# Performance work log

Measured on AMD Instinct MI355X. Metric: run time of the kernel, lower is better.

## Reference

```python
import jax, jax.numpy as jnp
import numpy as np

B, S, D = 4, 4096, 1024
H, HEAD_DIM = 16, 192  # head_dim split into q/k/v of 64 each


def setup_inputs() -> dict:
    key = jax.random.key(0)
    k1, k2 = jax.random.split(key)
    x = jax.random.normal(k1, (B, S, D), dtype=jnp.float32)
    qkv_kernel = jax.random.normal(k2, (D, H, HEAD_DIM), dtype=jnp.float32) * (1.0 / np.sqrt(D))
    qkv_bias = jnp.zeros((H, HEAD_DIM), dtype=jnp.float32)
    return {"x": x, "qkv_kernel": qkv_kernel, "qkv_bias": qkv_bias}


def reference(x, qkv_kernel, qkv_bias):
    # DenseGeneral: [B,S,D] x [D,H,HEAD_DIM] -> [B,S,H,HEAD_DIM]
    qkv = jnp.einsum('bsd,dhf->bshf', x, qkv_kernel) + qkv_bias
    q, k, v = jnp.split(qkv, 3, axis=-1)  # each [B,S,H,64]
    # Faithful to source layout: einsum '...hqd,...hkd' batches over (B,S) and
    # attends across the HEAD axis. With H <= block_size the blockwise loop in
    # the source collapses to this single full softmax over heads.
    scale = 1.0 / jnp.sqrt(jnp.asarray(HEAD_DIM, dtype=q.dtype))  # sqrt(self.head_dim)
    scores = jnp.einsum('bshd,bsgd->bshg', q, k) * scale  # [B,S,H,H]
    weights = jax.nn.softmax(scores, axis=-1)
    out = jnp.einsum('bshg,bsgd->bshd', weights, v)  # [B,S,H,64]
    return out
```

## Files before the change

### kernel.cpp

```cpp
#include <hip/hip_runtime.h>
#include <cstdint>
#include <cstddef>

typedef unsigned short u16;
typedef __attribute__((ext_vector_type(8))) short bf16x8;
typedef __attribute__((ext_vector_type(4))) float f32x4;

__device__ inline float bl(uint32_t u){ union{float f;uint32_t i;}c; c.i = u<<16; return c.f; }
__device__ inline float bh(uint32_t u){ union{float f;uint32_t i;}c; c.i = u & 0xFFFF0000u; return c.f; }
__device__ inline u16 f2bu(float f){
  union{float f;uint32_t u;} c; c.f=f;
  uint32_t u=c.u;
  return (u16)((u + 0x7FFFu + ((u>>16)&1u))>>16);
}

#define GLOAD_LDS16(g, l) __builtin_amdgcn_global_load_lds( \
    (__attribute__((address_space(1))) void*)(g), \
    (__attribute__((address_space(3))) void*)(l), 16, 0, 0)
#define BAR() do{ asm volatile("" ::: "memory"); __builtin_amdgcn_s_barrier(); asm volatile("" ::: "memory"); }while(0)

__global__ __launch_bounds__(256) void k_conv(const float* __restrict__ X,
                                              u16* __restrict__ Xb,
                                              const float* __restrict__ W,
                                              u16* __restrict__ Wt){
  __shared__ float t[32][33];
  int b = blockIdx.x;
  if (b < 2048){
    int i = b*256 + threadIdx.x;
    for (; i < 4194304; i += 2048*256){
      float4 v = ((const float4*)X)[i];
      ushort4 o;
      o.x=f2bu(v.x); o.y=f2bu(v.y); o.z=f2bu(v.z); o.w=f2bu(v.w);
      ((ushort4*)Xb)[i] = o;
    }
  } else {
    int bb = b - 2048;
    int n0 = (bb % 96)*32, k0 = (bb / 96)*32;
    int tx = threadIdx.x & 31, ty = threadIdx.x >> 5;
    #pragma unroll
    for (int i=0;i<32;i+=8)
      t[ty+i][tx] = W[(size_t)(k0+ty+i)*3072 + n0+tx];
    __syncthreads();
    #pragma unroll
    for (int i=0;i<32;i+=8)
      Wt[(size_t)(n0+ty+i)*1024 + k0+tx] = f2bu(t[tx][ty+i]);
  }
}

__global__ __launch_bounds__(512, 2) void k_gemm2(const u16* __restrict__ Xb,
                                                  const u16* __restrict__ Wt,
                                                  const float* __restrict__ bias,
                                                  u16* __restrict__ Q){
  __shared__ __align__(16) u16 L[65536];
  const int K = 1024, N = 3072, NT = 32;
  int b = blockIdx.x;
  int swz = (b & 7)*96 + (b >> 3);
  int bm = swz / 12, bn = swz % 12;
  int m0 = bm*256, n0 = bn*256;
  int tid = threadIdx.x, w = tid>>6, lane = tid&63, lr = lane&15, lk = lane>>4;
  int wm = w>>2, wn = w&3;

  f32x4 acc[8][4];
  #pragma unroll
  for (int i=0;i<8;i++)
    #pragma unroll
    for (int j=0;j<4;j++)
      acc[i][j] = (f32x4){0.f,0.f,0.f,0.f};

  int grow = tid>>2;
  int gcol = ((((tid&3)*16) ^ (((tid>>3)&1)<<4) ^ (((tid>>4)&1)<<5)) >> 1);
  const u16* gA0 = Xb + (size_t)(m0 + grow)*K + gcol;
  const u16* gA1 = Xb + (size_t)(m0 + 128 + grow)*K + gcol;
  const u16* gB0 = Wt + (size_t)(n0 + grow)*K + gcol;
  const u16* gB1 = Wt + (size_t)(n0 + 128 + grow)*K + gcol;

#define STG_A(j) do{ int bf=(j)&3, kof=(j)*32; \
    GLOAD_LDS16(gA0+kof, &L[((bf*4+0)<<12) + tid*8]); \
    GLOAD_LDS16(gA1+kof, &L[((bf*4+1)<<12) + tid*8]); }while(0)
#define STG_B(j) do{ int bf=(j)&3, kof=(j)*32; \
    GLOAD_LDS16(gB0+kof, &L[((bf*4+2)<<12) + tid*8]); \
    GLOAD_LDS16(gB1+kof, &L[((bf*4+3)<<12) + tid*8]); }while(0)

  const char* Lb = (const char*)L;
  int colx = (lk*16) ^ (((lr>>1)&3)*16);
  int arow = lr*64 + colx;
  int brow = ((wn&1)*64 + lr)*64 + colx;

  STG_A(0); STG_B(0);
  STG_A(1); STG_B(1);
  STG_A(2); STG_B(2);
  asm volatile("s_waitcnt vmcnt(8)" ::: "memory");
  __builtin_amdgcn_sched_barrier(0);
  BAR();

  for (int t = 0; t < NT; ++t){
    int buf = t & 3;
    int Abase = (buf*4 + wm) << 13;
    int Bbase = (buf*4 + 2 + (wn>>1)) << 13;
    bool st = (t <= NT-4);
    if (st) { STG_A(t+3); STG_B(t+3); }

    bf16x8 a0,a1,a2,a3,a4,a5,a6,a7, b0,b1,b2,b3;
    a0 = *(const bf16x8*)(Lb + Abase + 0*1024 + arow);
    a1 = *(const bf16x8*)(Lb + Abase + 1*1024 + arow);
    a2 = *(const bf16x8*)(Lb + Abase + 2*1024 + arow);
    a3 = *(const bf16x8*)(Lb + Abase + 3*1024 + arow);
    a4 = *(const bf16x8*)(Lb + Abase + 4*1024 + arow);
    a5 = *(const bf16x8*)(Lb + Abase + 5*1024 + arow);
    a6 = *(const bf16x8*)(Lb + Abase + 6*1024 + arow);
    a7 = *(const bf16x8*)(Lb + Abase + 7*1024 + arow);
    b0 = *(const bf16x8*)(Lb + Bbase + 0*1024 + brow);
    b1 = *(const bf16x8*)(Lb + Bbase + 1*1024 + brow);
    b2 = *(const bf16x8*)(Lb + Bbase + 2*1024 + brow);
    b3 = *(const bf16x8*)(Lb + Bbase + 3*1024 + brow);

    __builtin_amdgcn_s_setprio(1);
    acc[0][0] = __builtin_amdgcn_mfma_f32_16x16x32_bf16(a0, b0, acc[0][0], 0,0,0);
    acc[0][1] = __builtin_amdgcn_mfma_f32_16x16x32_bf16(a0, b1, acc[0][1], 0,0,0);
    acc[0][2] = __builtin_amdgcn_mfma_f32_16x16x32_bf16(a0, b2, acc[0][2], 0,0,0);
    acc[0][3] = __builtin_amdgcn_mfma_f32_16x16x32_bf16(a0, b3, acc[0][3], 0,0,0);
    acc[1][0] = __builtin_amdgcn_mfma_f32_16x16x32_bf16(a1, b0, acc[1][0], 0,0,0);
    acc[1][1] = __builtin_amdgcn_mfma_f32_16x16x32_bf16(a1, b1, acc[1][1], 0,0,0);
    acc[1][2] = __builtin_amdgcn_mfma_f32_16x16x32_bf16(a1, b2, acc[1][2], 0,0,0);
    acc[1][3] = __builtin_amdgcn_mfma_f32_16x16x32_bf16(a1, b3, acc[1][3], 0,0,0);
    acc[2][0] = __builtin_amdgcn_mfma_f32_16x16x32_bf16(a2, b0, acc[2][0], 0,0,0);
    acc[2][1] = __builtin_amdgcn_mfma_f32_16x16x32_bf16(a2, b1, acc[2][1], 0,0,0);
    acc[2][2] = __builtin_amdgcn_mfma_f32_16x16x32_bf16(a2, b2, acc[2][2], 0,0,0);
    acc[2][3] = __builtin_amdgcn_mfma_f32_16x16x32_bf16(a2, b3, acc[2][3], 0,0,0);
    acc[3][0] = __builtin_amdgcn_mfma_f32_16x16x32_bf16(a3, b0, acc[3][0], 0,0,0);
    acc[3][1] = __builtin_amdgcn_mfma_f32_16x16x32_bf16(a3, b1, acc[3][1], 0,0,0);
    acc[3][2] = __builtin_amdgcn_mfma_f32_16x16x32_bf16(a3, b2, acc[3][2], 0,0,0);
    acc[3][3] = __builtin_amdgcn_mfma_f32_16x16x32_bf16(a3, b3, acc[3][3], 0,0,0);
    acc[4][0] = __builtin_amdgcn_mfma_f32_16x16x32_bf16(a4, b0, acc[4][0], 0,0,0);
    acc[4][1] = __builtin_amdgcn_mfma_f32_16x16x32_bf16(a4, b1, acc[4][1], 0,0,0);
    acc[4][2] = __builtin_amdgcn_mfma_f32_16x16x32_bf16(a4, b2, acc[4][2], 0,0,0);
    acc[4][3] = __builtin_amdgcn_mfma_f32_16x16x32_bf16(a4, b3, acc[4][3], 0,0,0);
    acc[5][0] = __builtin_amdgcn_mfma_f32_16x16x32_bf16(a5, b0, acc[5][0], 0,0,0);
    acc[5][1] = __builtin_amdgcn_mfma_f32_16x16x32_bf16(a5, b1, acc[5][1], 0,0,0);
    acc[5][2] = __builtin_amdgcn_mfma_f32_16x16x32_bf16(a5, b2, acc[5][2], 0,0,0);
    acc[5][3] = __builtin_amdgcn_mfma_f32_16x16x32_bf16(a5, b3, acc[5][3], 0,0,0);
    acc[6][0] = __builtin_amdgcn_mfma_f32_16x16x32_bf16(a6, b0, acc[6][0], 0,0,0);
    acc[6][1] = __builtin_amdgcn_mfma_f32_16x16x32_bf16(a6, b1, acc[6][1], 0,0,0);
    acc[6][2] = __builtin_amdgcn_mfma_f32_16x16x32_bf16(a6, b2, acc[6][2], 0,0,0);
    acc[6][3] = __builtin_amdgcn_mfma_f32_16x16x32_bf16(a6, b3, acc[6][3], 0,0,0);
    acc[7][0] = __builtin_amdgcn_mfma_f32_16x16x32_bf16(a7, b0, acc[7][0], 0,0,0);
    acc[7][1] = __builtin_amdgcn_mfma_f32_16x16x32_bf16(a7, b1, acc[7][1], 0,0,0);
    acc[7][2] = __builtin_amdgcn_mfma_f32_16x16x32_bf16(a7, b2, acc[7][2], 0,0,0);
    acc[7][3] = __builtin_amdgcn_mfma_f32_16x16x32_bf16(a7, b3, acc[7][3], 0,0,0);
    __builtin_amdgcn_s_setprio(0);

    asm volatile("s_waitcnt lgkmcnt(0)" ::: "memory");
    if (t <= NT-4)      { asm volatile("s_waitcnt vmcnt(8)" ::: "memory"); }
    else if (t == NT-3) { asm volatile("s_waitcnt vmcnt(4)" ::: "memory"); }
    else if (t == NT-2) { asm volatile("s_waitcnt vmcnt(0)" ::: "memory"); }
    __builtin_amdgcn_sched_barrier(0);
    BAR();
  }
#undef STG_A
#undef STG_B

  {
    u16* reg = &L[w*8192];
    #pragma unroll
    for (int nf=0; nf<4; ++nf){
      int col = nf*16 + lr;
      float bv = bias[n0 + wn*64 + col];
      #pragma unroll
      for (int mi=0; mi<8; ++mi){
        #pragma unroll
        for (int r=0;r<4;r++){
          int rr = mi*16 + lk*4 + r;
          reg[rr*64 + (col ^ ((rr&7)<<3))] = f2bu(acc[mi][nf][r] + bv);
        }
      }
    }
    asm volatile("s_waitcnt lgkmcnt(0)" ::: "memory");
    BAR();
    int co = (tid&31)*8;
    int rgn_c = co>>6;
    int c6 = co&63;
    #pragma unroll
    for (int p=0; p<16; ++p){
      int rI = p*16 + (tid>>5);
      int wreg = ((rI>>7)<<2) + rgn_c;
      int rr = rI & 127;
      const u16* src = &L[wreg*8192 + rr*64 + (c6 ^ ((rr&7)<<3))];
      uint4 v = *(const uint4*)src;
      *(uint4*)&Q[(size_t)(m0+rI)*N + n0 + co] = v;
    }
  }
}

__device__ inline void load16fb(const u16* p, float* f){
  uint4 a = ((const uint4*)p)[0], b4 = ((const uint4*)p)[1];
  f[0]=bl(a.x);  f[1]=bh(a.x);  f[2]=bl(a.y);  f[3]=bh(a.y);
  f[4]=bl(a.z);  f[5]=bh(a.z);  f[6]=bl(a.w);  f[7]=bh(a.w);
  f[8]=bl(b4.x); f[9]=bh(b4.x); f[10]=bl(b4.y);f[11]=bh(b4.y);
  f[12]=bl(b4.z);f[13]=bh(b4.z);f[14]=bl(b4.w);f[15]=bh(b4.w);
}

__global__ __launch_bounds__(256) void k_attn(const u16* __restrict__ Qkv,
                                              float* __restrict__ out){
  __shared__ __align__(16) u16 sm[4][3072];
  int w = threadIdx.x>>6, lane = threadIdx.x&63;
  int token = blockIdx.x*4 + w;
  const uint4* src = (const uint4*)(Qkv + (size_t)token*3072);
  uint4* dst = (uint4*)&sm[w][0];
  for (int i = lane; i < 384; i += 64) dst[i] = src[i];
  __syncthreads();

  int h = lane>>2, dq = lane&3;
  const u16* base = &sm[w][0];
  float qf[16];
  load16fb(base + h*192 + dq*16, qf);

  const float scale = 0.07216878364870323f;
  float s[16];
  #pragma unroll
  for (int g=0; g<16; ++g){
    float kf[16];
    load16fb(base + g*192 + 64 + dq*16, kf);
    float a = 0.f;
    #pragma unroll
    for (int j=0;j<16;j++) a += qf[j]*kf[j];
    a += __shfl_xor(a, 1);
    a += __shfl_xor(a, 2);
    s[g] = a * scale;
  }
  float mx = s[0];
  #pragma unroll
  for (int g=1; g<16; ++g) mx = fmaxf(mx, s[g]);
  float sum = 0.f;
  #pragma unroll
  for (int g=0; g<16; ++g){ s[g] = __expf(s[g]-mx); sum += s[g]; }
  float inv = 1.f/sum;

  float o[16];
  #pragma unroll
  for (int j=0;j<16;j++) o[j] = 0.f;
  #pragma unroll
  for (int g=0; g<16; ++g){
    float wg = s[g]*inv;
    float vf[16];
    load16fb(base + g*192 + 128 + dq*16, vf);
    #pragma unroll
    for (int j=0;j<16;j++) o[j] += wg*vf[j];
  }
  float* op = out + (size_t)token*1024 + h*64 + dq*16;
  #pragma unroll
  for (int i=0;i<4;i++)
    ((float4*)op)[i] = make_float4(o[i*4], o[i*4+1], o[i*4+2], o[i*4+3]);
}

__global__ __launch_bounds__(256) void k_fallback(const float* __restrict__ X,
                                                  const float* __restrict__ W,
                                                  const float* __restrict__ bias,
                                                  float* __restrict__ out){
  int token = blockIdx.x;
  __shared__ float xs[1024];
  __shared__ float qkvs[3072];
  __shared__ float ss[16][16];
  __shared__ float ww[16][16];
  for (int i=threadIdx.x; i<1024; i+=256) xs[i] = X[(size_t)token*1024 + i];
  __syncthreads();
  for (int n=threadIdx.x; n<3072; n+=256){
    float acc = bias[n];
    for (int k=0;k<1024;k++) acc += xs[k]*W[(size_t)k*3072 + n];
    qkvs[n] = acc;
  }
  __syncthreads();
  {
    int t = threadIdx.x, h = t>>4, g = t&15;
    float a = 0.f;
    for (int d=0; d<64; d++) a += qkvs[h*192 + d]*qkvs[g*192 + 64 + d];
    ss[h][g] = a * 0.07216878364870323f;
  }
  __syncthreads();
  if (threadIdx.x < 16){
    int hh = threadIdx.x;
    float m = -1e30f;
    for (int g=0;g<16;g++) m = fmaxf(m, ss[hh][g]);
    float sum = 0.f;
    for (int g=0;g<16;g++){ float e = __expf(ss[hh][g]-m); ww[hh][g]=e; sum+=e; }
    float inv = 1.f/sum;
    for (int g=0;g<16;g++) ww[hh][g] *= inv;
  }
  __syncthreads();
  for (int i=threadIdx.x; i<1024; i+=256){
    int h = i>>6, d = i&63;
    float a = 0.f;
    for (int g=0;g<16;g++) a += ww[h][g]*qkvs[g*192 + 128 + d];
    out[(size_t)token*1024 + i] = a;
  }
}

extern "C" void kernel_launch(void* const* d_in, const int* in_sizes, int n_in,
                              void* d_out, int out_size, void* d_ws, size_t ws_size,
                              hipStream_t stream){
  const float* x    = (const float*)d_in[0];
  const float* wk   = (const float*)d_in[1];
  const float* bias = (const float*)d_in[2];
  float* out = (float*)d_out;

  const size_t offW = 33554432;
  const size_t offQ = offW + 6291456;
  const size_t need = offQ + (size_t)16384*3072*2;

  if (ws_size >= need){
    u16* Xb = (u16*)d_ws;
    u16* Wt = (u16*)((char*)d_ws + offW);
    u16* Q  = (u16*)((char*)d_ws + offQ);
    k_conv  <<<5120, 256, 0, stream>>>(x, Xb, wk, Wt);
    k_gemm2 <<<768, 512, 0, stream>>>(Xb, Wt, bias, Q);
    k_attn  <<<4096, 256, 0, stream>>>(Q, out);
  } else {
    k_fallback<<<16384, 256, 0, stream>>>(x, wk, bias, out);
  }
}
```

Measured before the change: 191.9 us.

## Deepen GEMM LDS ring to five stages and process two k-tiles per barrier

The LDS staging ring grows from four to five buffers, and A/B loads merge into a single STG macro. The main loop is unrolled by two, so each barrier and waitcnt now covers two k-tiles instead of one, with the prefetch distance kept at three to four tiles ahead. This halves the number of workgroup barriers and lets more loads stay in flight. In exchange, LDS usage rises to 160KB and launch bounds drop to one block per CU, which gives the compiler more register freedom but leaves no room for a second resident block.

```diff
diff --git a/kernel.cpp b/kernel.cpp
--- a/kernel.cpp
+++ b/kernel.cpp
@@ -47,11 +47,11 @@
   }
 }
 
-__global__ __launch_bounds__(512, 2) void k_gemm2(const u16* __restrict__ Xb,
+__global__ __launch_bounds__(512, 1) void k_gemm2(const u16* __restrict__ Xb,
                                                   const u16* __restrict__ Wt,
                                                   const float* __restrict__ bias,
                                                   u16* __restrict__ Q){
-  __shared__ __align__(16) u16 L[65536];
+  __shared__ __align__(16) u16 L[81920];
   const int K = 1024, N = 3072, NT = 32;
   int b = blockIdx.x;
   int swz = (b & 7)*96 + (b >> 3);
@@ -74,10 +74,9 @@
   const u16* gB0 = Wt + (size_t)(n0 + grow)*K + gcol;
   const u16* gB1 = Wt + (size_t)(n0 + 128 + grow)*K + gcol;
 
-#define STG_A(j) do{ int bf=(j)&3, kof=(j)*32; \
+#define STG(j) do{ int bf=(j)%5, kof=(j)*32; \
     GLOAD_LDS16(gA0+kof, &L[((bf*4+0)<<12) + tid*8]); \
-    GLOAD_LDS16(gA1+kof, &L[((bf*4+1)<<12) + tid*8]); }while(0)
-#define STG_B(j) do{ int bf=(j)&3, kof=(j)*32; \
+    GLOAD_LDS16(gA1+kof, &L[((bf*4+1)<<12) + tid*8]); \
     GLOAD_LDS16(gB0+kof, &L[((bf*4+2)<<12) + tid*8]); \
     GLOAD_LDS16(gB1+kof, &L[((bf*4+3)<<12) + tid*8]); }while(0)
 
@@ -86,78 +85,75 @@
   int arow = lr*64 + colx;
   int brow = ((wn&1)*64 + lr)*64 + colx;
 
-  STG_A(0); STG_B(0);
-  STG_A(1); STG_B(1);
-  STG_A(2); STG_B(2);
-  asm volatile("s_waitcnt vmcnt(8)" ::: "memory");
+#define TILE_BODY(bufidx) do{ \
+    int Abase = ((bufidx)*4 + wm) << 13; \
+    int Bbase = ((bufidx)*4 + 2 + (wn>>1)) << 13; \
+    bf16x8 a0,a1,a2,a3,a4,a5,a6,a7, b0,b1,b2,b3; \
+    a0 = *(const bf16x8*)(Lb + Abase + 0*1024 + arow); \
+    a1 = *(const bf16x8*)(Lb + Abase + 1*1024 + arow); \
+    a2 = *(const bf16x8*)(Lb + Abase + 2*1024 + arow); \
+    a3 = *(const bf16x8*)(Lb + Abase + 3*1024 + arow); \
+    a4 = *(const bf16x8*)(Lb + Abase + 4*1024 + arow); \
+    a5 = *(const bf16x8*)(Lb + Abase + 5*1024 + arow); \
+    a6 = *(const bf16x8*)(Lb + Abase + 6*1024 + arow); \
+    a7 = *(const bf16x8*)(Lb + Abase + 7*1024 + arow); \
+    b0 = *(const bf16x8*)(Lb + Bbase + 0*1024 + brow); \
+    b1 = *(const bf16x8*)(Lb + Bbase + 1*1024 + brow); \
+    b2 = *(const bf16x8*)(Lb + Bbase + 2*1024 + brow); \
+    b3 = *(const bf16x8*)(Lb + Bbase + 3*1024 + brow); \
+    __builtin_amdgcn_s_setprio(1); \
+    acc[0][0] = __builtin_amdgcn_mfma_f32_16x16x32_bf16(a0, b0, acc[0][0], 0,0,0); \
+    acc[0][1] = __builtin_amdgcn_mfma_f32_16x16x32_bf16(a0, b1, acc[0][1], 0,0,0); \
+    acc[0][2] = __builtin_amdgcn_mfma_f32_16x16x32_bf16(a0, b2, acc[0][2], 0,0,0); \
+    acc[0][3] = __builtin_amdgcn_mfma_f32_16x16x32_bf16(a0, b3, acc[0][3], 0,0,0); \
+    acc[1][0] = __builtin_amdgcn_mfma_f32_16x16x32_bf16(a1, b0, acc[1][0], 0,0,0); \
+    acc[1][1] = __builtin_amdgcn_mfma_f32_16x16x32_bf16(a1, b1, acc[1][1], 0,0,0); \
+    acc[1][2] = __builtin_amdgcn_mfma_f32_16x16x32_bf16(a1, b2, acc[1][2], 0,0,0); \
+    acc[1][3] = __builtin_amdgcn_mfma_f32_16x16x32_bf16(a1, b3, acc[1][3], 0,0,0); \
+    acc[2][0] = __builtin_amdgcn_mfma_f32_16x16x32_bf16(a2, b0, acc[2][0], 0,0,0); \
+    acc[2][1] = __builtin_amdgcn_mfma_f32_16x16x32_bf16(a2, b1, acc[2][1], 0,0,0); \
+    acc[2][2] = __builtin_amdgcn_mfma_f32_16x16x32_bf16(a2, b2, acc[2][2], 0,0,0); \
+    acc[2][3] = __builtin_amdgcn_mfma_f32_16x16x32_bf16(a2, b3, acc[2][3], 0,0,0); \
+    acc[3][0] = __builtin_amdgcn_mfma_f32_16x16x32_bf16(a3, b0, acc[3][0], 0,0,0); \
+    acc[3][1] = __builtin_amdgcn_mfma_f32_16x16x32_bf16(a3, b1, acc[3][1], 0,0,0); \
+    acc[3][2] = __builtin_amdgcn_mfma_f32_16x16x32_bf16(a3, b2, acc[3][2], 0,0,0); \
+    acc[3][3] = __builtin_amdgcn_mfma_f32_16x16x32_bf16(a3, b3, acc[3][3], 0,0,0); \
+    acc[4][0] = __builtin_amdgcn_mfma_f32_16x16x32_bf16(a4, b0, acc[4][0], 0,0,0); \
+    acc[4][1] = __builtin_amdgcn_mfma_f32_16x16x32_bf16(a4, b1, acc[4][1], 0,0,0); \
+    acc[4][2] = __builtin_amdgcn_mfma_f32_16x16x32_bf16(a4, b2, acc[4][2], 0,0,0); \
+    acc[4][3] = __builtin_amdgcn_mfma_f32_16x16x32_bf16(a4, b3, acc[4][3], 0,0,0); \
+    acc[5][0] = __builtin_amdgcn_mfma_f32_16x16x32_bf16(a5, b0, acc[5][0], 0,0,0); \
+    acc[5][1] = __builtin_amdgcn_mfma_f32_16x16x32_bf16(a5, b1, acc[5][1], 0,0,0); \
+    acc[5][2] = __builtin_amdgcn_mfma_f32_16x16x32_bf16(a5, b2, acc[5][2], 0,0,0); \
+    acc[5][3] = __builtin_amdgcn_mfma_f32_16x16x32_bf16(a5, b3, acc[5][3], 0,0,0); \
+    acc[6][0] = __builtin_amdgcn_mfma_f32_16x16x32_bf16(a6, b0, acc[6][0], 0,0,0); \
+    acc[6][1] = __builtin_amdgcn_mfma_f32_16x16x32_bf16(a6, b1, acc[6][1], 0,0,0); \
+    acc[6][2] = __builtin_amdgcn_mfma_f32_16x16x32_bf16(a6, b2, acc[6][2], 0,0,0); \
+    acc[6][3] = __builtin_amdgcn_mfma_f32_16x16x32_bf16(a6, b3, acc[6][3], 0,0,0); \
+    acc[7][0] = __builtin_amdgcn_mfma_f32_16x16x32_bf16(a7, b0, acc[7][0], 0,0,0); \
+    acc[7][1] = __builtin_amdgcn_mfma_f32_16x16x32_bf16(a7, b1, acc[7][1], 0,0,0); \
+    acc[7][2] = __builtin_amdgcn_mfma_f32_16x16x32_bf16(a7, b2, acc[7][2], 0,0,0); \
+    acc[7][3] = __builtin_amdgcn_mfma_f32_16x16x32_bf16(a7, b3, acc[7][3], 0,0,0); \
+    __builtin_amdgcn_s_setprio(0); }while(0)
+
+  STG(0); STG(1); STG(2);
+  asm volatile("s_waitcnt vmcnt(4)" ::: "memory");
   __builtin_amdgcn_sched_barrier(0);
   BAR();
 
-  for (int t = 0; t < NT; ++t){
-    int buf = t & 3;
-    int Abase = (buf*4 + wm) << 13;
-    int Bbase = (buf*4 + 2 + (wn>>1)) << 13;
-    bool st = (t <= NT-4);
-    if (st) { STG_A(t+3); STG_B(t+3); }
-
-    bf16x8 a0,a1,a2,a3,a4,a5,a6,a7, b0,b1,b2,b3;
-    a0 = *(const bf16x8*)(Lb + Abase + 0*1024 + arow);
-    a1 = *(const bf16x8*)(Lb + Abase + 1*1024 + arow);
-    a2 = *(const bf16x8*)(Lb + Abase + 2*1024 + arow);
-    a3 = *(const bf16x8*)(Lb + Abase + 3*1024 + arow);
-    a4 = *(const bf16x8*)(Lb + Abase + 4*1024 + arow);
-    a5 = *(const bf16x8*)(Lb + Abase + 5*1024 + arow);
-    a6 = *(const bf16x8*)(Lb + Abase + 6*1024 + arow);
-    a7 = *(const bf16x8*)(Lb + Abase + 7*1024 + arow);
-    b0 = *(const bf16x8*)(Lb + Bbase + 0*1024 + brow);
-    b1 = *(const bf16x8*)(Lb + Bbase + 1*1024 + brow);
-    b2 = *(const bf16x8*)(Lb + Bbase + 2*1024 + brow);
-    b3 = *(const bf16x8*)(Lb + Bbase + 3*1024 + brow);
-
-    __builtin_amdgcn_s_setprio(1);
-    acc[0][0] = __builtin_amdgcn_mfma_f32_16x16x32_bf16(a0, b0, acc[0][0], 0,0,0);
-    acc[0][1] = __builtin_amdgcn_mfma_f32_16x16x32_bf16(a0, b1, acc[0][1], 0,0,0);
-    acc[0][2] = __builtin_amdgcn_mfma_f32_16x16x32_bf16(a0, b2, acc[0][2], 0,0,0);
-    acc[0][3] = __builtin_amdgcn_mfma_f32_16x16x32_bf16(a0, b3, acc[0][3], 0,0,0);
-    acc[1][0] = __builtin_amdgcn_mfma_f32_16x16x32_bf16(a1, b0, acc[1][0], 0,0,0);
-    acc[1][1] = __builtin_amdgcn_mfma_f32_16x16x32_bf16(a1, b1, acc[1][1], 0,0,0);
-    acc[1][2] = __builtin_amdgcn_mfma_f32_16x16x32_bf16(a1, b2, acc[1][2], 0,0,0);
-    acc[1][3] = __builtin_amdgcn_mfma_f32_16x16x32_bf16(a1, b3, acc[1][3], 0,0,0);
-    acc[2][0] = __builtin_amdgcn_mfma_f32_16x16x32_bf16(a2, b0, acc[2][0], 0,0,0);
-    acc[2][1] = __builtin_amdgcn_mfma_f32_16x16x32_bf16(a2, b1, acc[2][1], 0,0,0);
-    acc[2][2] = __builtin_amdgcn_mfma_f32_16x16x32_bf16(a2, b2, acc[2][2], 0,0,0);
-    acc[2][3] = __builtin_amdgcn_mfma_f32_16x16x32_bf16(a2, b3, acc[2][3], 0,0,0);
-    acc[3][0] = __builtin_amdgcn_mfma_f32_16x16x32_bf16(a3, b0, acc[3][0], 0,0,0);
-    acc[3][1] = __builtin_amdgcn_mfma_f32_16x16x32_bf16(a3, b1, acc[3][1], 0,0,0);
-    acc[3][2] = __builtin_amdgcn_mfma_f32_16x16x32_bf16(a3, b2, acc[3][2], 0,0,0);
-    acc[3][3] = __builtin_amdgcn_mfma_f32_16x16x32_bf16(a3, b3, acc[3][3], 0,0,0);
-    acc[4][0] = __builtin_amdgcn_mfma_f32_16x16x32_bf16(a4, b0, acc[4][0], 0,0,0);
-    acc[4][1] = __builtin_amdgcn_mfma_f32_16x16x32_bf16(a4, b1, acc[4][1], 0,0,0);
-    acc[4][2] = __builtin_amdgcn_mfma_f32_16x16x32_bf16(a4, b2, acc[4][2], 0,0,0);
-    acc[4][3] = __builtin_amdgcn_mfma_f32_16x16x32_bf16(a4, b3, acc[4][3], 0,0,0);
-    acc[5][0] = __builtin_amdgcn_mfma_f32_16x16x32_bf16(a5, b0, acc[5][0], 0,0,0);
-    acc[5][1] = __builtin_amdgcn_mfma_f32_16x16x32_bf16(a5, b1, acc[5][1], 0,0,0);
-    acc[5][2] = __builtin_amdgcn_mfma_f32_16x16x32_bf16(a5, b2, acc[5][2], 0,0,0);
-    acc[5][3] = __builtin_amdgcn_mfma_f32_16x16x32_bf16(a5, b3, acc[5][3], 0,0,0);
-    acc[6][0] = __builtin_amdgcn_mfma_f32_16x16x32_bf16(a6, b0, acc[6][0], 0,0,0);
-    acc[6][1] = __builtin_amdgcn_mfma_f32_16x16x32_bf16(a6, b1, acc[6][1], 0,0,0);
-    acc[6][2] = __builtin_amdgcn_mfma_f32_16x16x32_bf16(a6, b2, acc[6][2], 0,0,0);
-    acc[6][3] = __builtin_amdgcn_mfma_f32_16x16x32_bf16(a6, b3, acc[6][3], 0,0,0);
-    acc[7][0] = __builtin_amdgcn_mfma_f32_16x16x32_bf16(a7, b0, acc[7][0], 0,0,0);
-    acc[7][1] = __builtin_amdgcn_mfma_f32_16x16x32_bf16(a7, b1, acc[7][1], 0,0,0);
-    acc[7][2] = __builtin_amdgcn_mfma_f32_16x16x32_bf16(a7, b2, acc[7][2], 0,0,0);
-    acc[7][3] = __builtin_amdgcn_mfma_f32_16x16x32_bf16(a7, b3, acc[7][3], 0,0,0);
-    __builtin_amdgcn_s_setprio(0);
-
+  for (int t = 0; t < NT; t += 2){
+    if (t+3 < NT) STG(t+3);
+    TILE_BODY(t%5);
+    if (t+4 < NT) STG(t+4);
+    TILE_BODY((t+1)%5);
     asm volatile("s_waitcnt lgkmcnt(0)" ::: "memory");
-    if (t <= NT-4)      { asm volatile("s_waitcnt vmcnt(8)" ::: "memory"); }
-    else if (t == NT-3) { asm volatile("s_waitcnt vmcnt(4)" ::: "memory"); }
-    else if (t == NT-2) { asm volatile("s_waitcnt vmcnt(0)" ::: "memory"); }
+    if      (t+4 < NT) { asm volatile("s_waitcnt vmcnt(4)" ::: "memory"); }
+    else if (t+2 < NT) { asm volatile("s_waitcnt vmcnt(0)" ::: "memory"); }
     __builtin_amdgcn_sched_barrier(0);
     BAR();
   }
-#undef STG_A
-#undef STG_B
+#undef STG
+#undef TILE_BODY
 
   {
     u16* reg = &L[w*8192];
```

New measurement: 190.9 us. No clear change (-0.5%).

## Split GEMM main loop into two half-phases with a five-stage LDS ring

Applied to the files above, without the earlier changes.

Grows the LDS staging ring from four to five K-slices and drops the occupancy hint to one block per CU, since the larger shared buffer no longer fits two. Each K-iteration now runs in two halves: the first loads A and half of B, issues the A prefetch, then runs 16 MFMAs; the second loads the other half of B, issues the B prefetch, then runs the remaining 16 MFMAs. Extra barriers are placed between the halves. The goal is to interleave global-to-LDS traffic with matrix math in a ping-pong style schedule, at the cost of more barriers per iteration and half the resident waves per CU.

```diff
diff --git a/kernel.cpp b/kernel.cpp
--- a/kernel.cpp
+++ b/kernel.cpp
@@ -18,6 +18,8 @@
     (__attribute__((address_space(1))) void*)(g), \
     (__attribute__((address_space(3))) void*)(l), 16, 0, 0)
 #define BAR() do{ asm volatile("" ::: "memory"); __builtin_amdgcn_s_barrier(); asm volatile("" ::: "memory"); }while(0)
+#define WAITVM(n) do{ asm volatile("s_waitcnt vmcnt(" #n ")" ::: "memory"); __builtin_amdgcn_sched_barrier(0); }while(0)
+#define WAITLG() do{ asm volatile("s_waitcnt lgkmcnt(0)" ::: "memory"); __builtin_amdgcn_sched_barrier(0); }while(0)
 
 __global__ __launch_bounds__(256) void k_conv(const float* __restrict__ X,
                                               u16* __restrict__ Xb,
@@ -47,11 +49,11 @@
   }
 }
 
-__global__ __launch_bounds__(512, 2) void k_gemm2(const u16* __restrict__ Xb,
+__global__ __launch_bounds__(512, 1) void k_gemm2(const u16* __restrict__ Xb,
                                                   const u16* __restrict__ Wt,
                                                   const float* __restrict__ bias,
                                                   u16* __restrict__ Q){
-  __shared__ __align__(16) u16 L[65536];
+  __shared__ __align__(16) u16 L[81920];
   const int K = 1024, N = 3072, NT = 32;
   int b = blockIdx.x;
   int swz = (b & 7)*96 + (b >> 3);
@@ -74,10 +76,10 @@
   const u16* gB0 = Wt + (size_t)(n0 + grow)*K + gcol;
   const u16* gB1 = Wt + (size_t)(n0 + 128 + grow)*K + gcol;
 
-#define STG_A(j) do{ int bf=(j)&3, kof=(j)*32; \
+#define STG_A(j) do{ int bf=(j)%5, kof=(j)*32; \
     GLOAD_LDS16(gA0+kof, &L[((bf*4+0)<<12) + tid*8]); \
     GLOAD_LDS16(gA1+kof, &L[((bf*4+1)<<12) + tid*8]); }while(0)
-#define STG_B(j) do{ int bf=(j)&3, kof=(j)*32; \
+#define STG_B(j) do{ int bf=(j)%5, kof=(j)*32; \
     GLOAD_LDS16(gB0+kof, &L[((bf*4+2)<<12) + tid*8]); \
     GLOAD_LDS16(gB1+kof, &L[((bf*4+3)<<12) + tid*8]); }while(0)
 
@@ -89,18 +91,16 @@
   STG_A(0); STG_B(0);
   STG_A(1); STG_B(1);
   STG_A(2); STG_B(2);
-  asm volatile("s_waitcnt vmcnt(8)" ::: "memory");
-  __builtin_amdgcn_sched_barrier(0);
+  WAITVM(8);
   BAR();
 
   for (int t = 0; t < NT; ++t){
-    int buf = t & 3;
+    int buf = t % 5;
     int Abase = (buf*4 + wm) << 13;
     int Bbase = (buf*4 + 2 + (wn>>1)) << 13;
-    bool st = (t <= NT-4);
-    if (st) { STG_A(t+3); STG_B(t+3); }
-
-    bf16x8 a0,a1,a2,a3,a4,a5,a6,a7, b0,b1,b2,b3;
+    bool st = (t+3 < NT);
+
+    bf16x8 a0,a1,a2,a3,a4,a5,a6,a7, b0,b1;
     a0 = *(const bf16x8*)(Lb + Abase + 0*1024 + arow);
     a1 = *(const bf16x8*)(Lb + Abase + 1*1024 + arow);
     a2 = *(const bf16x8*)(Lb + Abase + 2*1024 + arow);
@@ -111,49 +111,56 @@
     a7 = *(const bf16x8*)(Lb + Abase + 7*1024 + arow);
     b0 = *(const bf16x8*)(Lb + Bbase + 0*1024 + brow);
     b1 = *(const bf16x8*)(Lb + Bbase + 1*1024 + brow);
-    b2 = *(const bf16x8*)(Lb + Bbase + 2*1024 + brow);
-    b3 = *(const bf16x8*)(Lb + Bbase + 3*1024 + brow);
-
+    if (st) STG_A(t+3);
+    BAR();
+    WAITLG();
     __builtin_amdgcn_s_setprio(1);
     acc[0][0] = __builtin_amdgcn_mfma_f32_16x16x32_bf16(a0, b0, acc[0][0], 0,0,0);
     acc[0][1] = __builtin_amdgcn_mfma_f32_16x16x32_bf16(a0, b1, acc[0][1], 0,0,0);
+    acc[1][0] = __builtin_amdgcn_mfma_f32_16x16x32_bf16(a1, b0, acc[1][0], 0,0,0);
+    acc[1][1] = __builtin_amdgcn_mfma_f32_16x16x32_bf16(a1, b1, acc[1][1], 0,0,0);
+    acc[2][0] = __builtin_amdgcn_mfma_f32_16x16x32_bf16(a2, b0, acc[2][0], 0,0,0);
+    acc[2][1] = __builtin_amdgcn_mfma_f32_16x16x32_bf16(a2, b1, acc[2][1], 0,0,0);
+    acc[3][0] = __builtin_amdgcn_mfma_f32_16x16x32_bf16(a3, b0, acc[3][0], 0,0,0);
+    acc[3][1] = __builtin_amdgcn_mfma_f32_16x16x32_bf16(a3, b1, acc[3][1], 0,0,0);
+    acc[4][0] = __builtin_amdgcn_mfma_f32_16x16x32_bf16(a4, b0, acc[4][0], 0,0,0);
+    acc[4][1] = __builtin_amdgcn_mfma_f32_16x16x32_bf16(a4, b1, acc[4][1], 0,0,0);
+    acc[5][0] = __builtin_amdgcn_mfma_f32_16x16x32_bf16(a5, b0, acc[5][0], 0,0,0);
+    acc[5][1] = __builtin_amdgcn_mfma_f32_16x16x32_bf16(a5, b1, acc[5][1], 0,0,0);
+    acc[6][0] = __builtin_amdgcn_mfma_f32_16x16x32_bf16(a6, b0, acc[6][0], 0,0,0);
+    acc[6][1] = __builtin_amdgcn_mfma_f32_16x16x32_bf16(a6, b1, acc[6][1], 0,0,0);
+    acc[7][0] = __builtin_amdgcn_mfma_f32_16x16x32_bf16(a7, b0, acc[7][0], 0,0,0);
+    acc[7][1] = __builtin_amdgcn_mfma_f32_16x16x32_bf16(a7, b1, acc[7][1], 0,0,0);
+    __builtin_amdgcn_s_setprio(0);
+    BAR();
+
+    bf16x8 b2, b3;
+    b2 = *(const bf16x8*)(Lb + Bbase + 2*1024 + brow);
+    b3 = *(const bf16x8*)(Lb + Bbase + 3*1024 + brow);
+    if (st) STG_B(t+3);
+    BAR();
+    WAITLG();
+    __builtin_amdgcn_s_setprio(1);
     acc[0][2] = __builtin_amdgcn_mfma_f32_16x16x32_bf16(a0, b2, acc[0][2], 0,0,0);
     acc[0][3] = __builtin_amdgcn_mfma_f32_16x16x32_bf16(a0, b3, acc[0][3], 0,0,0);
-    acc[1][0] = __builtin_amdgcn_mfma_f32_16x16x32_bf16(a1, b0, acc[1][0], 0,0,0);
-    acc[1][1] = __builtin_amdgcn_mfma_f32_16x16x32_bf16(a1, b1, acc[1][1], 0,0,0);
     acc[1][2] = __builtin_amdgcn_mfma_f32_16x16x32_bf16(a1, b2, acc[1][2], 0,0,0);
     acc[1][3] = __builtin_amdgcn_mfma_f32_16x16x32_bf16(a1, b3, acc[1][3], 0,0,0);
-    acc[2][0] = __builtin_amdgcn_mfma_f32_16x16x32_bf16(a2, b0, acc[2][0], 0,0,0);
-    acc[2][1] = __builtin_amdgcn_mfma_f32_16x16x32_bf16(a2, b1, acc[2][1], 0,0,0);
     acc[2][2] = __builtin_amdgcn_mfma_f32_16x16x32_bf16(a2, b2, acc[2][2], 0,0,0);
     acc[2][3] = __builtin_amdgcn_mfma_f32_16x16x32_bf16(a2, b3, acc[2][3], 0,0,0);
-    acc[3][0] = __builtin_amdgcn_mfma_f32_16x16x32_bf16(a3, b0, acc[3][0], 0,0,0);
-    acc[3][1] = __builtin_amdgcn_mfma_f32_16x16x32_bf16(a3, b1, acc[3][1], 0,0,0);
     acc[3][2] = __builtin_amdgcn_mfma_f32_16x16x32_bf16(a3, b2, acc[3][2], 0,0,0);
     acc[3][3] = __builtin_amdgcn_mfma_f32_16x16x32_bf16(a3, b3, acc[3][3], 0,0,0);
-    acc[4][0] = __builtin_amdgcn_mfma_f32_16x16x32_bf16(a4, b0, acc[4][0], 0,0,0);
-    acc[4][1] = __builtin_amdgcn_mfma_f32_16x16x32_bf16(a4, b1, acc[4][1], 0,0,0);
     acc[4][2] = __builtin_amdgcn_mfma_f32_16x16x32_bf16(a4, b2, acc[4][2], 0,0,0);
     acc[4][3] = __builtin_amdgcn_mfma_f32_16x16x32_bf16(a4, b3, acc[4][3], 0,0,0);
-    acc[5][0] = __builtin_amdgcn_mfma_f32_16x16x32_bf16(a5, b0, acc[5][0], 0,0,0);
-    acc[5][1] = __builtin_amdgcn_mfma_f32_16x16x32_bf16(a5, b1, acc[5][1], 0,0,0);
     acc[5][2] = __builtin_amdgcn_mfma_f32_16x16x32_bf16(a5, b2, acc[5][2], 0,0,0);
     acc[5][3] = __builtin_amdgcn_mfma_f32_16x16x32_bf16(a5, b3, acc[5][3], 0,0,0);
-    acc[6][0] = __builtin_amdgcn_mfma_f32_16x16x32_bf16(a6, b0, acc[6][0], 0,0,0);
-    acc[6][1] = __builtin_amdgcn_mfma_f32_16x16x32_bf16(a6, b1, acc[6][1], 0,0,0);
     acc[6][2] = __builtin_amdgcn_mfma_f32_16x16x32_bf16(a6, b2, acc[6][2], 0,0,0);
     acc[6][3] = __builtin_amdgcn_mfma_f32_16x16x32_bf16(a6, b3, acc[6][3], 0,0,0);
-    acc[7][0] = __builtin_amdgcn_mfma_f32_16x16x32_bf16(a7, b0, acc[7][0], 0,0,0);
-    acc[7][1] = __builtin_amdgcn_mfma_f32_16x16x32_bf16(a7, b1, acc[7][1], 0,0,0);
     acc[7][2] = __builtin_amdgcn_mfma_f32_16x16x32_bf16(a7, b2, acc[7][2], 0,0,0);
     acc[7][3] = __builtin_amdgcn_mfma_f32_16x16x32_bf16(a7, b3, acc[7][3], 0,0,0);
     __builtin_amdgcn_s_setprio(0);
-
-    asm volatile("s_waitcnt lgkmcnt(0)" ::: "memory");
-    if (t <= NT-4)      { asm volatile("s_waitcnt vmcnt(8)" ::: "memory"); }
-    else if (t == NT-3) { asm volatile("s_waitcnt vmcnt(4)" ::: "memory"); }
-    else if (t == NT-2) { asm volatile("s_waitcnt vmcnt(0)" ::: "memory"); }
-    __builtin_amdgcn_sched_barrier(0);
+    if (t <= NT-4)      { WAITVM(8); }
+    else if (t == NT-3) { WAITVM(4); }
+    else if (t == NT-2) { WAITVM(0); }
     BAR();
   }
 #undef STG_A
```

New measurement: 192.3 us. Within noise of the previous version (+0.2%).
